# Kernel tuning notes

Measured on AMD Instinct MI355X. Metric: run time of the kernel, lower is better.

Reference implementation:

```python
import jax, jax.numpy as jnp
import numpy as np

NORM_EPS = 1e-6


def setup_inputs() -> dict:
    key = jax.random.key(0)
    k1, k2 = jax.random.split(key)
    in_features, out_features = 4096, 4096
    x = jax.random.normal(k1, (2, 2048, in_features), dtype=jnp.float32)
    scale = 1.0 / np.sqrt(in_features)
    weight = jax.random.normal(k2, (out_features, in_features), dtype=jnp.float32) * scale
    norm_weight = jnp.ones((in_features,), dtype=jnp.float32)
    return {"x": x, "weight": weight, "norm_weight": norm_weight}


def reference(x, weight, norm_weight):
    # RMSNorm over the last dim
    rms = jnp.sqrt(jnp.mean(x * x, axis=-1, keepdims=True) + NORM_EPS)
    x_n = x / rms * norm_weight
    # ternary weight quantization (absmean scale alpha)
    alpha = jnp.maximum(jnp.mean(jnp.abs(weight)), 1e-10)
    w_q = jnp.clip(jnp.round(weight / alpha), -1.0, 1.0)
    # per-token int8 activation quantization (absmax scale gamma)
    gamma = jnp.maximum(jnp.max(jnp.abs(x_n), axis=-1, keepdims=True), 1e-10)
    x_q = jnp.clip(jnp.round(x_n * 127.0 / gamma), -128.0, 127.0)
    # rescaled matmul: y = x_q @ w_q.T * (alpha * gamma / 127)
    y = jnp.einsum('bsk,nk->bsn', x_q, w_q) * (alpha * gamma / 127.0)
    return y
```

## Files before the change

### kernel.cpp

```cpp
#include <hip/hip_runtime.h>
#include <cstdint>
#include <cstddef>


#define KD 4096
#define MD 4096
#define ND 4096

typedef int i32x4 __attribute__((ext_vector_type(4)));


__global__ __launch_bounds__(256) void k_alpha_part(const float* __restrict__ w,
                                                    float* __restrict__ part) {
  __shared__ float red[256];
  const int tid = threadIdx.x;
  const float4* w4 = (const float4*)(w + (size_t)blockIdx.x * 4096);
  float s = 0.f;
#pragma unroll
  for (int i = 0; i < 4; ++i) {
    float4 v = w4[i * 256 + tid];
    s += fabsf(v.x) + fabsf(v.y) + fabsf(v.z) + fabsf(v.w);
  }
  red[tid] = s;
  __syncthreads();
  for (int st = 128; st > 0; st >>= 1) {
    if (tid < st) red[tid] += red[tid + st];
    __syncthreads();
  }
  if (tid == 0) part[blockIdx.x] = red[0];
}

__global__ __launch_bounds__(256) void k_alpha_final(const float* __restrict__ part,
                                                     float* __restrict__ alpha) {
  __shared__ float red[256];
  const int tid = threadIdx.x;
  float s = 0.f;
#pragma unroll
  for (int i = 0; i < 16; ++i) s += part[i * 256 + tid];
  red[tid] = s;
  __syncthreads();
  for (int st = 128; st > 0; st >>= 1) {
    if (tid < st) red[tid] += red[tid + st];
    __syncthreads();
  }
  if (tid == 0) alpha[0] = fmaxf(red[0] * (1.0f / 16777216.0f), 1e-10f);
}


__global__ __launch_bounds__(256) void k_quant_w(const float* __restrict__ w,
                                                 const float* __restrict__ alpha_p,
                                                 signed char* __restrict__ wq) {
  const float alpha = alpha_p[0];
  const int tid = threadIdx.x;
  const float4* w4 = (const float4*)(w + (size_t)blockIdx.x * 4096);
  uint32_t* wqi = (uint32_t*)(wq + (size_t)blockIdx.x * 4096);
#pragma unroll
  for (int i = 0; i < 4; ++i) {
    const int f = i * 256 + tid;
    float4 v = w4[f];
    int q0 = (int)fminf(fmaxf(rintf(v.x / alpha), -1.f), 1.f);
    int q1 = (int)fminf(fmaxf(rintf(v.y / alpha), -1.f), 1.f);
    int q2 = (int)fminf(fmaxf(rintf(v.z / alpha), -1.f), 1.f);
    int q3 = (int)fminf(fmaxf(rintf(v.w / alpha), -1.f), 1.f);
    wqi[f] = (uint32_t)(q0 & 255) | ((uint32_t)(q1 & 255) << 8) |
             ((uint32_t)(q2 & 255) << 16) | ((uint32_t)(q3 & 255) << 24);
  }
}


__global__ __launch_bounds__(256) void k_rmsnorm_quant(const float* __restrict__ x,
                                                       const float* __restrict__ nw,
                                                       signed char* __restrict__ xq,
                                                       float* __restrict__ gamma) {
  __shared__ float red[256];
  const int tid = threadIdx.x;
  const int row = blockIdx.x;
  const float4* x4 = (const float4*)(x + (size_t)row * 4096);
  const float4* n4 = (const float4*)nw;
  float4 xv[4], nv[4];
  float ss = 0.f;
#pragma unroll
  for (int i = 0; i < 4; ++i) {
    xv[i] = x4[i * 256 + tid];
    nv[i] = n4[i * 256 + tid];
    ss += xv[i].x * xv[i].x + xv[i].y * xv[i].y + xv[i].z * xv[i].z + xv[i].w * xv[i].w;
  }
  red[tid] = ss;
  __syncthreads();
  for (int st = 128; st > 0; st >>= 1) {
    if (tid < st) red[tid] += red[tid + st];
    __syncthreads();
  }
  const float rms = sqrtf(red[0] * (1.0f / 4096.0f) + 1e-6f);
  __syncthreads();

  float4 xn[4];
  float mx = 0.f;
#pragma unroll
  for (int i = 0; i < 4; ++i) {
    xn[i].x = xv[i].x / rms * nv[i].x;
    xn[i].y = xv[i].y / rms * nv[i].y;
    xn[i].z = xv[i].z / rms * nv[i].z;
    xn[i].w = xv[i].w / rms * nv[i].w;
    mx = fmaxf(mx, fmaxf(fmaxf(fabsf(xn[i].x), fabsf(xn[i].y)),
                         fmaxf(fabsf(xn[i].z), fabsf(xn[i].w))));
  }
  red[tid] = mx;
  __syncthreads();
  for (int st = 128; st > 0; st >>= 1) {
    if (tid < st) red[tid] = fmaxf(red[tid], red[tid + st]);
    __syncthreads();
  }
  const float g = fmaxf(red[0], 1e-10f);
  if (tid == 0) gamma[row] = g;

  uint32_t* xqi = (uint32_t*)(xq + (size_t)row * 4096);
#pragma unroll
  for (int i = 0; i < 4; ++i) {
    const int f = i * 256 + tid;
    int q0 = (int)fminf(fmaxf(rintf(xn[i].x * 127.0f / g), -128.f), 127.f);
    int q1 = (int)fminf(fmaxf(rintf(xn[i].y * 127.0f / g), -128.f), 127.f);
    int q2 = (int)fminf(fmaxf(rintf(xn[i].z * 127.0f / g), -128.f), 127.f);
    int q3 = (int)fminf(fmaxf(rintf(xn[i].w * 127.0f / g), -128.f), 127.f);
    xqi[f] = (uint32_t)(q0 & 255) | ((uint32_t)(q1 & 255) << 8) |
             ((uint32_t)(q2 & 255) << 16) | ((uint32_t)(q3 & 255) << 24);
  }
}


__global__ __launch_bounds__(256) void k_gemm(const signed char* __restrict__ xq,
                                              const signed char* __restrict__ wq,
                                              const float* __restrict__ gamma,
                                              const float* __restrict__ alpha_p,
                                              float* __restrict__ out) {
  __shared__ __align__(16) signed char As[128 * 64];
  __shared__ __align__(16) signed char Bs[128 * 64];
  const int tid = threadIdx.x;
  const int lane = tid & 63;
  const int wave = tid >> 6;
  const int wm = (wave >> 1) * 64;
  const int wn = (wave & 1) * 64;
  const int quad = lane >> 4;
  const int l16 = lane & 15;
  const int bm = blockIdx.y * 128;
  const int bn = blockIdx.x * 128;

  const signed char* Ag = xq + (size_t)bm * KD;
  const signed char* Bg = wq + (size_t)bn * KD;

  const int r0 = tid >> 2;
  const int c0 = (tid & 3) * 16;
  const signed char* agp0 = Ag + (size_t)r0 * KD + c0;
  const signed char* agp1 = Ag + (size_t)(r0 + 64) * KD + c0;
  const signed char* bgp0 = Bg + (size_t)r0 * KD + c0;
  const signed char* bgp1 = Bg + (size_t)(r0 + 64) * KD + c0;
  signed char* al0 = &As[r0 * 64 + c0];
  signed char* al1 = &As[(r0 + 64) * 64 + c0];
  signed char* bl0 = &Bs[r0 * 64 + c0];
  signed char* bl1 = &Bs[(r0 + 64) * 64 + c0];

  i32x4 acc[4][4];
#pragma unroll
  for (int i = 0; i < 4; ++i)
#pragma unroll
    for (int j = 0; j < 4; ++j) acc[i][j] = (i32x4){0, 0, 0, 0};

  for (int k0 = 0; k0 < KD; k0 += 64) {
    __syncthreads();
    *(i32x4*)al0 = *(const i32x4*)(agp0 + k0);
    *(i32x4*)al1 = *(const i32x4*)(agp1 + k0);
    *(i32x4*)bl0 = *(const i32x4*)(bgp0 + k0);
    *(i32x4*)bl1 = *(const i32x4*)(bgp1 + k0);
    __syncthreads();

    i32x4 af[4], bf[4];
#pragma unroll
    for (int mi = 0; mi < 4; ++mi)
      af[mi] = *(const i32x4*)&As[(wm + mi * 16 + l16) * 64 + quad * 16];
#pragma unroll
    for (int ni = 0; ni < 4; ++ni)
      bf[ni] = *(const i32x4*)&Bs[(wn + ni * 16 + l16) * 64 + quad * 16];
#pragma unroll
    for (int mi = 0; mi < 4; ++mi)
#pragma unroll
      for (int ni = 0; ni < 4; ++ni)
        acc[mi][ni] = __builtin_amdgcn_mfma_i32_16x16x64_i8(af[mi], bf[ni],
                                                            acc[mi][ni], 0, 0, 0);
  }

  const float alpha = alpha_p[0];
#pragma unroll
  for (int mi = 0; mi < 4; ++mi) {
#pragma unroll
    for (int r = 0; r < 4; ++r) {
      const int m = bm + wm + mi * 16 + quad * 4 + r;
      const float s = (alpha * gamma[m]) / 127.0f;
#pragma unroll
      for (int ni = 0; ni < 4; ++ni) {
        const int n = bn + wn + ni * 16 + l16;
        out[(size_t)m * ND + n] = (float)acc[mi][ni][r] * s;
      }
    }
  }
}


extern "C" void kernel_launch(void* const* d_in, const int* in_sizes, int n_in,
                              void* d_out, int out_size, void* d_ws, size_t ws_size,
                              hipStream_t stream) {
  const float* x = (const float*)d_in[0];
  const float* w = (const float*)d_in[1];
  const float* nw = (const float*)d_in[2];
  float* out = (float*)d_out;

  char* ws = (char*)d_ws;
  signed char* xq = (signed char*)ws;
  signed char* wq = (signed char*)(ws + ((size_t)1 << 24));
  float* gamma = (float*)(ws + ((size_t)2 << 24));
  float* part = (float*)(ws + ((size_t)2 << 24) + 16384);
  float* alpha = (float*)(ws + ((size_t)2 << 24) + 32768);

  k_alpha_part<<<4096, 256, 0, stream>>>(w, part);
  k_alpha_final<<<1, 256, 0, stream>>>(part, alpha);
  k_quant_w<<<4096, 256, 0, stream>>>(w, alpha, wq);
  k_rmsnorm_quant<<<4096, 256, 0, stream>>>(x, nw, xq, gamma);
  dim3 g(ND / 128, MD / 128);
  k_gemm<<<g, 256, 0, stream>>>(xq, wq, gamma, alpha, out);
}
```

Before: 281.1 us.

## Use direct global-to-LDS loads with XOR swizzle in GEMM; wave-shuffle reductions

The int8 GEMM now stages its A and B tiles with global_load_lds, which writes straight into shared memory without passing through registers. It also applies an XOR swizzle to the 16-byte chunks so the MFMA fragment reads avoid LDS bank conflicts. The block reductions in the alpha and RMSNorm kernels are replaced by wave shuffle reductions followed by a small 4-entry shared array, cutting barriers. The swizzle must match exactly between the store layout and the read addressing, and the GEMM is still single-buffered with no overlap between loads and compute.

```diff
diff --git a/kernel.cpp b/kernel.cpp
--- a/kernel.cpp
+++ b/kernel.cpp
@@ -9,10 +9,27 @@
 
 typedef int i32x4 __attribute__((ext_vector_type(4)));
 
+__device__ __forceinline__ void gl2lds16(const signed char* g, signed char* l) {
+  __builtin_amdgcn_global_load_lds(
+      (const __attribute__((address_space(1))) void*)g,
+      (__attribute__((address_space(3))) void*)l, 16, 0, 0);
+}
+
+__device__ __forceinline__ float wave_sum(float v) {
+#pragma unroll
+  for (int off = 32; off; off >>= 1) v += __shfl_down(v, off, 64);
+  return v;
+}
+__device__ __forceinline__ float wave_max(float v) {
+#pragma unroll
+  for (int off = 32; off; off >>= 1) v = fmaxf(v, __shfl_down(v, off, 64));
+  return v;
+}
+
 
 __global__ __launch_bounds__(256) void k_alpha_part(const float* __restrict__ w,
                                                     float* __restrict__ part) {
-  __shared__ float red[256];
+  __shared__ float red[4];
   const int tid = threadIdx.x;
   const float4* w4 = (const float4*)(w + (size_t)blockIdx.x * 4096);
   float s = 0.f;
@@ -21,29 +38,25 @@
     float4 v = w4[i * 256 + tid];
     s += fabsf(v.x) + fabsf(v.y) + fabsf(v.z) + fabsf(v.w);
   }
-  red[tid] = s;
-  __syncthreads();
-  for (int st = 128; st > 0; st >>= 1) {
-    if (tid < st) red[tid] += red[tid + st];
-    __syncthreads();
-  }
-  if (tid == 0) part[blockIdx.x] = red[0];
+  s = wave_sum(s);
+  if ((tid & 63) == 0) red[tid >> 6] = s;
+  __syncthreads();
+  if (tid == 0) part[blockIdx.x] = (red[0] + red[1]) + (red[2] + red[3]);
 }
 
 __global__ __launch_bounds__(256) void k_alpha_final(const float* __restrict__ part,
                                                      float* __restrict__ alpha) {
-  __shared__ float red[256];
+  __shared__ float red[4];
   const int tid = threadIdx.x;
   float s = 0.f;
 #pragma unroll
   for (int i = 0; i < 16; ++i) s += part[i * 256 + tid];
-  red[tid] = s;
-  __syncthreads();
-  for (int st = 128; st > 0; st >>= 1) {
-    if (tid < st) red[tid] += red[tid + st];
-    __syncthreads();
-  }
-  if (tid == 0) alpha[0] = fmaxf(red[0] * (1.0f / 16777216.0f), 1e-10f);
+  s = wave_sum(s);
+  if ((tid & 63) == 0) red[tid >> 6] = s;
+  __syncthreads();
+  if (tid == 0)
+    alpha[0] = fmaxf(((red[0] + red[1]) + (red[2] + red[3])) * (1.0f / 16777216.0f),
+                     1e-10f);
 }
 
 
@@ -72,7 +85,8 @@
                                                        const float* __restrict__ nw,
                                                        signed char* __restrict__ xq,
                                                        float* __restrict__ gamma) {
-  __shared__ float red[256];
+  __shared__ float red[4];
+  __shared__ float red2[4];
   const int tid = threadIdx.x;
   const int row = blockIdx.x;
   const float4* x4 = (const float4*)(x + (size_t)row * 4096);
@@ -85,14 +99,11 @@
     nv[i] = n4[i * 256 + tid];
     ss += xv[i].x * xv[i].x + xv[i].y * xv[i].y + xv[i].z * xv[i].z + xv[i].w * xv[i].w;
   }
-  red[tid] = ss;
-  __syncthreads();
-  for (int st = 128; st > 0; st >>= 1) {
-    if (tid < st) red[tid] += red[tid + st];
-    __syncthreads();
-  }
-  const float rms = sqrtf(red[0] * (1.0f / 4096.0f) + 1e-6f);
-  __syncthreads();
+  ss = wave_sum(ss);
+  if ((tid & 63) == 0) red[tid >> 6] = ss;
+  __syncthreads();
+  const float tot = (red[0] + red[1]) + (red[2] + red[3]);
+  const float rms = sqrtf(tot * (1.0f / 4096.0f) + 1e-6f);
 
   float4 xn[4];
   float mx = 0.f;
@@ -105,13 +116,11 @@
     mx = fmaxf(mx, fmaxf(fmaxf(fabsf(xn[i].x), fabsf(xn[i].y)),
                          fmaxf(fabsf(xn[i].z), fabsf(xn[i].w))));
   }
-  red[tid] = mx;
-  __syncthreads();
-  for (int st = 128; st > 0; st >>= 1) {
-    if (tid < st) red[tid] = fmaxf(red[tid], red[tid + st]);
-    __syncthreads();
-  }
-  const float g = fmaxf(red[0], 1e-10f);
+  mx = wave_max(mx);
+  if ((tid & 63) == 0) red2[tid >> 6] = mx;
+  __syncthreads();
+  const float g = fmaxf(fmaxf(fmaxf(red2[0], red2[1]), fmaxf(red2[2], red2[3])),
+                        1e-10f);
   if (tid == 0) gamma[row] = g;
 
   uint32_t* xqi = (uint32_t*)(xq + (size_t)row * 4096);
@@ -148,38 +157,41 @@
   const signed char* Ag = xq + (size_t)bm * KD;
   const signed char* Bg = wq + (size_t)bn * KD;
 
-  const int r0 = tid >> 2;
-  const int c0 = (tid & 3) * 16;
-  const signed char* agp0 = Ag + (size_t)r0 * KD + c0;
-  const signed char* agp1 = Ag + (size_t)(r0 + 64) * KD + c0;
-  const signed char* bgp0 = Bg + (size_t)r0 * KD + c0;
-  const signed char* bgp1 = Bg + (size_t)(r0 + 64) * KD + c0;
-  signed char* al0 = &As[r0 * 64 + c0];
-  signed char* al1 = &As[(r0 + 64) * 64 + c0];
-  signed char* bl0 = &Bs[r0 * 64 + c0];
-  signed char* bl1 = &Bs[(r0 + 64) * 64 + c0];
+  const int srow = wave * 16 + (lane >> 2);
+  const int schunk = (lane & 3) ^ ((lane >> 3) & 3);
+  const signed char* agp0 = Ag + (size_t)srow * KD + schunk * 16;
+  const signed char* agp1 = Ag + (size_t)(srow + 64) * KD + schunk * 16;
+  const signed char* bgp0 = Bg + (size_t)srow * KD + schunk * 16;
+  const signed char* bgp1 = Bg + (size_t)(srow + 64) * KD + schunk * 16;
+  signed char* la0 = &As[wave * 1024];
+  signed char* la1 = &As[4096 + wave * 1024];
+  signed char* lb0 = &Bs[wave * 1024];
+  signed char* lb1 = &Bs[4096 + wave * 1024];
 
   i32x4 acc[4][4];
 #pragma unroll
   for (int i = 0; i < 4; ++i)
 #pragma unroll
     for (int j = 0; j < 4; ++j) acc[i][j] = (i32x4){0, 0, 0, 0};
+
+  const int sw = (l16 >> 1) & 3;
+  const int apos = (quad ^ sw) * 16;
 
   for (int k0 = 0; k0 < KD; k0 += 64) {
     __syncthreads();
-    *(i32x4*)al0 = *(const i32x4*)(agp0 + k0);
-    *(i32x4*)al1 = *(const i32x4*)(agp1 + k0);
-    *(i32x4*)bl0 = *(const i32x4*)(bgp0 + k0);
-    *(i32x4*)bl1 = *(const i32x4*)(bgp1 + k0);
+    gl2lds16(agp0 + k0, la0);
+    gl2lds16(agp1 + k0, la1);
+    gl2lds16(bgp0 + k0, lb0);
+    gl2lds16(bgp1 + k0, lb1);
     __syncthreads();
 
     i32x4 af[4], bf[4];
 #pragma unroll
     for (int mi = 0; mi < 4; ++mi)
-      af[mi] = *(const i32x4*)&As[(wm + mi * 16 + l16) * 64 + quad * 16];
+      af[mi] = *(const i32x4*)&As[(wm + mi * 16 + l16) * 64 + apos];
 #pragma unroll
     for (int ni = 0; ni < 4; ++ni)
-      bf[ni] = *(const i32x4*)&Bs[(wn + ni * 16 + l16) * 64 + quad * 16];
+      bf[ni] = *(const i32x4*)&Bs[(wn + ni * 16 + l16) * 64 + apos];
 #pragma unroll
     for (int mi = 0; mi < 4; ++mi)
 #pragma unroll
```

Measured after the change: 269.9 us. -4.0%, faster.
